# Performance work log

Measured on AMD Instinct MI355X. Metric: run time of the kernel, lower is better.

## Reference

```python
import jax, jax.numpy as jnp
import numpy as np

EPS = 1e-4  # BatchNorm2d eps from source


def binarize(x):
    # brevitas 1-bit quant: sign(x) with sign(0)=+1; straight-through (clipped) estimator
    y = jnp.clip(x, -1.0, 1.0)
    q = jnp.where(x >= 0, 1.0, -1.0).astype(x.dtype)
    return y + jax.lax.stop_gradient(q - y)


def bn(x, g, b, m, v):
    inv = g / jnp.sqrt(v + EPS)
    return x * inv[None, :, None, None] + (b - m * inv)[None, :, None, None]


def conv(x, w, pad):
    return jax.lax.conv_general_dilated(
        x, w, window_strides=(1, 1), padding=[(pad, pad), (pad, pad)],
        dimension_numbers=('NCHW', 'OIHW', 'NCHW'))


def conv_mod(x, w1, bn1, w3, bn3):
    # conv1x1(binary W) -> BN -> binarize act -> conv3x3(binary W) -> BN -> binarize act
    x = conv(x, binarize(w1), 0)
    x = binarize(bn(x, *bn1))
    x = conv(x, binarize(w3), 1)
    x = binarize(bn(x, *bn3))
    return x


def maxpool2(x):
    return jax.lax.reduce_window(x, -jnp.inf, jax.lax.max,
                                 (1, 1, 2, 2), (1, 1, 2, 2), 'VALID')


def setup_inputs() -> dict:
    key = jax.random.key(0)
    ks = jax.random.split(key, 24)
    B, Cin, down, up, H, W = 16, 256, 64, 256, 56, 56
    d = {
        'x':   jax.random.normal(ks[0], (B, Cin, H, W), jnp.float32),
        'w11': jax.random.normal(ks[1], (down, Cin, 1, 1), jnp.float32) * 0.1,
        'w31': jax.random.normal(ks[2], (up, down, 3, 3), jnp.float32) * 0.1,
        'w12': jax.random.normal(ks[3], (down, up, 1, 1), jnp.float32) * 0.1,
        'w32': jax.random.normal(ks[4], (up, down, 3, 3), jnp.float32) * 0.1,
    }
    # BatchNorm params (inference stats): gamma, beta, running mean, running var
    for i, (tag, c) in enumerate([('11', down), ('31', up), ('12', down), ('32', up)]):
        d['g' + tag] = jax.random.uniform(ks[5 + 4 * i], (c,), jnp.float32, 0.5, 1.5)
        d['b' + tag] = jax.random.normal(ks[6 + 4 * i], (c,), jnp.float32) * 0.1
        d['m' + tag] = jax.random.normal(ks[7 + 4 * i], (c,), jnp.float32) * 0.1
        d['v' + tag] = jax.random.uniform(ks[8 + 4 * i], (c,), jnp.float32, 0.5, 1.5)
    return d


def reference(x, w11, w31, w12, w32,
              g11, b11, m11, v11, g31, b31, m31, v31,
              g12, b12, m12, v12, g32, b32, m32, v32):
    h = conv_mod(x, w11, (g11, b11, m11, v11), w31, (g31, b31, m31, v31))
    r = conv_mod(h, w12, (g12, b12, m12, v12), w32, (g32, b32, m32, v32))
    s = binarize(h + r)          # quant_add: re-binarize the residual sum
    return maxpool2(s)           # MaxPool2d(2)
```

## Files before the change

### kernel.cpp

```cpp
#include <hip/hip_runtime.h>
#include <stdint.h>

#pragma clang fp contract(off)


#define HW_   3136
#define NPIX  50176

#define OFF_W31B   0
#define OFF_W12B   18432
#define OFF_W32B   20480
#define OFF_IV11   38912
#define OFF_IV31   39424
#define OFF_IV12   41472
#define OFF_IV32   41984
#define OFF_SGNT   44032
#define OFF_A1     109568
#define OFF_A2     510976
#define OFF_H      912384
#define OFF_S      2518016

__device__ inline float2 mk_ivbt(float g, float b, float m, float v) {
    float inv  = __fdiv_rn(g, __fsqrt_rn(__fadd_rn(v, 1e-4f)));
    float beta = __fsub_rn(b, __fmul_rn(m, inv));
    return make_float2(inv, beta);
}

__global__ __launch_bounds__(256) void k0_all(
    const float* __restrict__ w11, const float* __restrict__ w31,
    const float* __restrict__ w12, const float* __restrict__ w32,
    const float* __restrict__ g11, const float* __restrict__ b11,
    const float* __restrict__ m11, const float* __restrict__ v11,
    const float* __restrict__ g31, const float* __restrict__ b31,
    const float* __restrict__ m31, const float* __restrict__ v31,
    const float* __restrict__ g12, const float* __restrict__ b12,
    const float* __restrict__ m12, const float* __restrict__ v12,
    const float* __restrict__ g32, const float* __restrict__ b32,
    const float* __restrict__ m32, const float* __restrict__ v32,
    uint64_t* __restrict__ W31b, uint64_t* __restrict__ W12b,
    uint64_t* __restrict__ W32b,
    float2* __restrict__ iv11, float2* __restrict__ iv31,
    float2* __restrict__ iv12, float2* __restrict__ iv32,
    float* __restrict__ sgnT)
{
    int blk = blockIdx.x;
    if (blk < 1216) {
        int wid = blk * 4 + (threadIdx.x >> 6);
        int l = threadIdx.x & 63;
        if (wid < 2304) {
            int co = wid / 9, tap = wid % 9;
            uint64_t bits = __ballot(w31[(co * 64 + l) * 9 + tap] >= 0.f);
            if (l == 0) W31b[wid] = bits;
        } else if (wid < 4608) {
            int i = wid - 2304;
            int co = i / 9, tap = i % 9;
            uint64_t bits = __ballot(w32[(co * 64 + l) * 9 + tap] >= 0.f);
            if (l == 0) W32b[i] = bits;
        } else if (wid < 4864) {
            int i = wid - 4608;
            int co = i >> 2, k = i & 3;
            uint64_t bits = __ballot(w12[co * 256 + k * 64 + l] >= 0.f);
            if (l == 0) W12b[i] = bits;
        }
    } else if (blk < 1219) {
        int i = (blk - 1216) * 256 + threadIdx.x;
        if (i < 64)        iv11[i]       = mk_ivbt(g11[i],       b11[i],       m11[i],       v11[i]);
        else if (i < 320)  iv31[i - 64]  = mk_ivbt(g31[i - 64],  b31[i - 64],  m31[i - 64],  v31[i - 64]);
        else if (i < 384)  iv12[i - 320] = mk_ivbt(g12[i - 320], b12[i - 320], m12[i - 320], v12[i - 320]);
        else if (i < 640)  iv32[i - 384] = mk_ivbt(g32[i - 384], b32[i - 384], m32[i - 384], v32[i - 384]);
    } else {
        int t = (blk - 1219) * 256 + threadIdx.x;
        int j = t >> 8, ci = t & 255;
        sgnT[ci * 64 + j] = (w11[t] >= 0.f) ? 1.0f : -1.0f;
    }
}

__global__ __launch_bounds__(256) void k1_conv1(
    const float* __restrict__ x, const float* __restrict__ sgnT,
    const float2* __restrict__ ivbt, unsigned char* __restrict__ A1)
{
    const int l = threadIdx.x & 63;
    const int wv = __builtin_amdgcn_readfirstlane(threadIdx.x >> 6);
    const int blk = blockIdx.x;
    const int half = blk & 1;
    const int g = half * 4 + wv;
    const int P = (blk >> 1) * 256 + l * 4;
    const int bl = P / HW_;
    const int pxl = P - bl * HW_;
    const float* xp = x + (size_t)bl * (256 * HW_) + pxl;
    const float* sg = sgnT + g * 8;

    float acc[8][4];
#pragma unroll
    for (int j = 0; j < 8; ++j)
#pragma unroll
        for (int p = 0; p < 4; ++p) acc[j][p] = 0.0f;

    for (int ci = 0; ci < 256; ci += 8) {
        float4 xv[8];
#pragma unroll
        for (int k = 0; k < 8; ++k)
            xv[k] = *(const float4*)(xp + (size_t)(ci + k) * HW_);
#pragma unroll
        for (int k = 0; k < 8; ++k) {
            const float* s = sg + (ci + k) * 64;
#pragma unroll
            for (int j = 0; j < 8; ++j) {
                acc[j][0] = __builtin_fmaf(s[j], xv[k].x, acc[j][0]);
                acc[j][1] = __builtin_fmaf(s[j], xv[k].y, acc[j][1]);
                acc[j][2] = __builtin_fmaf(s[j], xv[k].z, acc[j][2]);
                acc[j][3] = __builtin_fmaf(s[j], xv[k].w, acc[j][3]);
            }
        }
    }

    unsigned bp0 = 0, bp1 = 0, bp2 = 0, bp3 = 0;
#pragma unroll
    for (int j = 0; j < 8; ++j) {
        float2 ib = ivbt[g * 8 + j];
        bp0 |= (__fadd_rn(__fmul_rn(acc[j][0], ib.x), ib.y) >= 0.0f) ? (1u << j) : 0u;
        bp1 |= (__fadd_rn(__fmul_rn(acc[j][1], ib.x), ib.y) >= 0.0f) ? (1u << j) : 0u;
        bp2 |= (__fadd_rn(__fmul_rn(acc[j][2], ib.x), ib.y) >= 0.0f) ? (1u << j) : 0u;
        bp3 |= (__fadd_rn(__fmul_rn(acc[j][3], ib.x), ib.y) >= 0.0f) ? (1u << j) : 0u;
    }
    unsigned char* a = A1 + (size_t)P * 8 + g;
    a[0]  = (unsigned char)bp0;
    a[8]  = (unsigned char)bp1;
    a[16] = (unsigned char)bp2;
    a[24] = (unsigned char)bp3;
}

template <bool MERGE, bool DO_K3>
__global__ __launch_bounds__(256) void k_conv3c(
    const uint64_t* __restrict__ A, const uint64_t* __restrict__ Wb,
    const float2* __restrict__ ivbt, const uint64_t* __restrict__ Hin,
    uint64_t* __restrict__ Out,
    const uint64_t* __restrict__ W12b, const float2* __restrict__ iv12,
    unsigned short* __restrict__ A2)
{
    __shared__ uint64_t tile[4 * 58];
    __shared__ uint64_t sh4[4][64];
    const int l = threadIdx.x & 63;
    const int wv = threadIdx.x >> 6;
    const int wvu = __builtin_amdgcn_readfirstlane(wv);
    const int chunk = blockIdx.x;
    const int b = chunk / 49;
    const int hw0 = (chunk % 49) * 64;
    const int r0 = hw0 / 56;
    const int o  = hw0 % 56;
    const int rfirst = r0 - 1;

    {
        int idx = threadIdx.x;
        if (idx < 4 * 58) {
            int rr = idx / 58, cc = idx % 58;
            int gh = rfirst + rr, gw = cc - 1;
            uint64_t v = 0;
            if ((unsigned)gh < 56u && (unsigned)gw < 56u)
                v = A[b * HW_ + gh * 56 + gw];
            tile[idx] = v;
        }
    }
    __syncthreads();

    const int inrow2 = (l >= 56 - o) ? 1 : 0;
    const int w = o + l - (inrow2 ? 56 : 0);
    const int row = r0 + inrow2;
    const int rbase = inrow2 * 58;

    uint64_t a[9], m[9];
    int nv = 0;
#pragma unroll
    for (int dr = 0; dr < 3; ++dr)
#pragma unroll
        for (int dc = 0; dc < 3; ++dc) {
            int t = dr * 3 + dc;
            a[t] = tile[rbase + dr * 58 + w + dc];
            bool ok = ((unsigned)(row + dr - 1) < 56u) &&
                      ((unsigned)(w + dc - 1) < 56u);
            m[t] = ok ? ~0ull : 0ull;
            nv += ok;
        }
    const int base = 64 * nv;

    const uint64_t* wbase = Wb + wvu * 64 * 9;
    const float2*   ivb   = ivbt + wvu * 64;

    uint64_t bits = 0;
#pragma unroll 4
    for (int jo = 0; jo < 64; ++jo) {
        const uint64_t* wq = wbase + jo * 9;
        int s = 0;
#pragma unroll
        for (int t = 0; t < 9; ++t)
            s += (int)__popcll((a[t] ^ wq[t]) & m[t]);
        int y = base - 2 * s;
        float2 ib = ivb[jo];
        float val = __fadd_rn(__fmul_rn((float)y, ib.x), ib.y);
        bits |= (uint64_t)(val >= 0.0f) << jo;
    }

    size_t oidx = (size_t)wv * NPIX + (size_t)(b * HW_) + hw0 + l;
    if (MERGE) bits |= Hin[oidx];
    Out[oidx] = bits;

    if (DO_K3) {
        sh4[wv][l] = bits;
        __syncthreads();
        uint64_t h0 = sh4[0][l], h1 = sh4[1][l], h2 = sh4[2][l], h3 = sh4[3][l];
        unsigned bits16 = 0;
#pragma unroll
        for (int jj = 0; jj < 16; ++jj) {
            int cq = wvu * 16 + jj;
            const uint64_t* wq = W12b + cq * 4;
            int s = (int)(__popcll(h0 ^ wq[0]) + __popcll(h1 ^ wq[1]) +
                          __popcll(h2 ^ wq[2]) + __popcll(h3 ^ wq[3]));
            int y = 256 - 2 * s;
            float2 ibq = iv12[cq];
            float val = __fadd_rn(__fmul_rn((float)y, ibq.x), ibq.y);
            bits16 |= (val >= 0.0f) ? (1u << jj) : 0u;
        }
        A2[(size_t)(b * HW_ + hw0 + l) * 4 + wv] = (unsigned short)bits16;
    }
}

__global__ __launch_bounds__(256) void k4b_pool(
    const uint64_t* __restrict__ S, float* __restrict__ out)
{
    int o = blockIdx.x * 256 + threadIdx.x;
    int ow = o % 28;
    int t = o / 28;
    int oh = t % 28; t /= 28;
    int co = t & 255;
    int b  = t >> 8;
    int k = co >> 6, j = co & 63;
    const uint64_t* Sk = S + (size_t)k * NPIX + (size_t)(b * HW_) + (2 * oh) * 56 + 2 * ow;
    uint64_t s = Sk[0] | Sk[1] | Sk[56] | Sk[57];
    out[o] = ((s >> j) & 1) ? 1.0f : -1.0f;
}

extern "C" void kernel_launch(void* const* d_in, const int* in_sizes, int n_in,
                              void* d_out, int out_size, void* d_ws, size_t ws_size,
                              hipStream_t stream)
{
    const float* x   = (const float*)d_in[0];
    const float* w11 = (const float*)d_in[1];
    const float* w31 = (const float*)d_in[2];
    const float* w12 = (const float*)d_in[3];
    const float* w32 = (const float*)d_in[4];
    const float* g11 = (const float*)d_in[5];
    const float* b11 = (const float*)d_in[6];
    const float* m11 = (const float*)d_in[7];
    const float* v11 = (const float*)d_in[8];
    const float* g31 = (const float*)d_in[9];
    const float* b31 = (const float*)d_in[10];
    const float* m31 = (const float*)d_in[11];
    const float* v31 = (const float*)d_in[12];
    const float* g12 = (const float*)d_in[13];
    const float* b12 = (const float*)d_in[14];
    const float* m12 = (const float*)d_in[15];
    const float* v12 = (const float*)d_in[16];
    const float* g32 = (const float*)d_in[17];
    const float* b32 = (const float*)d_in[18];
    const float* m32 = (const float*)d_in[19];
    const float* v32 = (const float*)d_in[20];

    char* ws = (char*)d_ws;
    uint64_t* W31b = (uint64_t*)(ws + OFF_W31B);
    uint64_t* W12b = (uint64_t*)(ws + OFF_W12B);
    uint64_t* W32b = (uint64_t*)(ws + OFF_W32B);
    float2* iv11 = (float2*)(ws + OFF_IV11);
    float2* iv31 = (float2*)(ws + OFF_IV31);
    float2* iv12 = (float2*)(ws + OFF_IV12);
    float2* iv32 = (float2*)(ws + OFF_IV32);
    float*  sgnT = (float*)(ws + OFF_SGNT);
    uint64_t* A1 = (uint64_t*)(ws + OFF_A1);
    uint64_t* A2 = (uint64_t*)(ws + OFF_A2);
    uint64_t* Hb = (uint64_t*)(ws + OFF_H);
    uint64_t* Sb = (uint64_t*)(ws + OFF_S);

    k0_all<<<dim3(1283), dim3(256), 0, stream>>>(
        w11, w31, w12, w32,
        g11, b11, m11, v11, g31, b31, m31, v31,
        g12, b12, m12, v12, g32, b32, m32, v32,
        W31b, W12b, W32b, iv11, iv31, iv12, iv32, sgnT);

    k1_conv1<<<dim3(392), dim3(256), 0, stream>>>(x, sgnT, iv11, (unsigned char*)A1);

    k_conv3c<false, true><<<dim3(784), dim3(256), 0, stream>>>(
        A1, W31b, iv31, (const uint64_t*)nullptr, Hb,
        W12b, iv12, (unsigned short*)A2);

    k_conv3c<true, false><<<dim3(784), dim3(256), 0, stream>>>(
        A2, W32b, iv32, Hb, Sb,
        (const uint64_t*)nullptr, (const float2*)nullptr, (unsigned short*)nullptr);

    k4b_pool<<<dim3(12544), dim3(256), 0, stream>>>(Sb, (float*)d_out);
}
```

Baseline: 116.0 us.

## Retile conv1x1 kernel to 32 channels x 2 pixels per thread with double-buffered loads

The 1x1 binary-weight conv kernel now has each thread compute 32 output channels for 2 pixels instead of 8 channels for 4 pixels. Blocks shrink to 128 threads (two waves, each covering half of the 64 output channels), which removes the duplicate reads of x across blocks. Channel loads are software-pipelined with two register buffers to overlap memory with FMAs, and results are written as 32-bit words instead of bytes. The larger per-thread accumulator set and launch_bounds(128,1) raise register use, and the grid keeps 392 blocks of only 2 waves each, so GPU occupancy drops sharply.

```diff
diff --git a/kernel.cpp b/kernel.cpp
--- a/kernel.cpp
+++ b/kernel.cpp
@@ -75,59 +75,61 @@
     }
 }
 
-__global__ __launch_bounds__(256) void k1_conv1(
+__global__ __launch_bounds__(128, 1) void k1_conv1(
     const float* __restrict__ x, const float* __restrict__ sgnT,
-    const float2* __restrict__ ivbt, unsigned char* __restrict__ A1)
+    const float2* __restrict__ ivbt, uint32_t* __restrict__ A1)
 {
     const int l = threadIdx.x & 63;
-    const int wv = __builtin_amdgcn_readfirstlane(threadIdx.x >> 6);
+    const int half = __builtin_amdgcn_readfirstlane(threadIdx.x >> 6);
     const int blk = blockIdx.x;
-    const int half = blk & 1;
-    const int g = half * 4 + wv;
-    const int P = (blk >> 1) * 256 + l * 4;
+    const int P = blk * 128 + l * 2;
     const int bl = P / HW_;
     const int pxl = P - bl * HW_;
     const float* xp = x + (size_t)bl * (256 * HW_) + pxl;
-    const float* sg = sgnT + g * 8;
-
-    float acc[8][4];
-#pragma unroll
-    for (int j = 0; j < 8; ++j)
-#pragma unroll
-        for (int p = 0; p < 4; ++p) acc[j][p] = 0.0f;
-
-    for (int ci = 0; ci < 256; ci += 8) {
-        float4 xv[8];
-#pragma unroll
-        for (int k = 0; k < 8; ++k)
-            xv[k] = *(const float4*)(xp + (size_t)(ci + k) * HW_);
-#pragma unroll
-        for (int k = 0; k < 8; ++k) {
-            const float* s = sg + (ci + k) * 64;
-#pragma unroll
-            for (int j = 0; j < 8; ++j) {
-                acc[j][0] = __builtin_fmaf(s[j], xv[k].x, acc[j][0]);
-                acc[j][1] = __builtin_fmaf(s[j], xv[k].y, acc[j][1]);
-                acc[j][2] = __builtin_fmaf(s[j], xv[k].z, acc[j][2]);
-                acc[j][3] = __builtin_fmaf(s[j], xv[k].w, acc[j][3]);
-            }
-        }
-    }
-
-    unsigned bp0 = 0, bp1 = 0, bp2 = 0, bp3 = 0;
-#pragma unroll
-    for (int j = 0; j < 8; ++j) {
-        float2 ib = ivbt[g * 8 + j];
+    const float* sg = sgnT + half * 32;
+
+    float acc[32][2];
+#pragma unroll
+    for (int j = 0; j < 32; ++j) { acc[j][0] = 0.0f; acc[j][1] = 0.0f; }
+
+    float2 bufA[8], bufB[8];
+
+#define PF(B, CI0)                                                          \
+    _Pragma("unroll")                                                       \
+    for (int k = 0; k < 8; ++k)                                             \
+        B[k] = *(const float2*)(xp + (size_t)((CI0) + k) * HW_);
+
+#define COMP(B, CI0)                                                        \
+    _Pragma("unroll")                                                       \
+    for (int k = 0; k < 8; ++k) {                                           \
+        const float* s_ = sg + ((CI0) + k) * 64;                            \
+        _Pragma("unroll")                                                   \
+        for (int j = 0; j < 32; ++j) {                                      \
+            acc[j][0] = __builtin_fmaf(s_[j], B[k].x, acc[j][0]);           \
+            acc[j][1] = __builtin_fmaf(s_[j], B[k].y, acc[j][1]);           \
+        }                                                                   \
+    }
+
+    PF(bufA, 0)
+    for (int cb = 0; cb < 256; cb += 16) {
+        PF(bufB, cb + 8)
+        COMP(bufA, cb)
+        if (cb + 16 < 256) { PF(bufA, cb + 16) }
+        COMP(bufB, cb + 8)
+    }
+#undef PF
+#undef COMP
+
+    uint32_t bp0 = 0, bp1 = 0;
+#pragma unroll
+    for (int j = 0; j < 32; ++j) {
+        float2 ib = ivbt[half * 32 + j];
         bp0 |= (__fadd_rn(__fmul_rn(acc[j][0], ib.x), ib.y) >= 0.0f) ? (1u << j) : 0u;
         bp1 |= (__fadd_rn(__fmul_rn(acc[j][1], ib.x), ib.y) >= 0.0f) ? (1u << j) : 0u;
-        bp2 |= (__fadd_rn(__fmul_rn(acc[j][2], ib.x), ib.y) >= 0.0f) ? (1u << j) : 0u;
-        bp3 |= (__fadd_rn(__fmul_rn(acc[j][3], ib.x), ib.y) >= 0.0f) ? (1u << j) : 0u;
-    }
-    unsigned char* a = A1 + (size_t)P * 8 + g;
-    a[0]  = (unsigned char)bp0;
-    a[8]  = (unsigned char)bp1;
-    a[16] = (unsigned char)bp2;
-    a[24] = (unsigned char)bp3;
+    }
+    uint32_t* a = A1 + (size_t)P * 2 + half;
+    a[0] = bp0;
+    a[2] = bp1;
 }
 
 template <bool MERGE, bool DO_K3>
@@ -285,7 +287,7 @@
         g12, b12, m12, v12, g32, b32, m32, v32,
         W31b, W12b, W32b, iv11, iv31, iv12, iv32, sgnT);
 
-    k1_conv1<<<dim3(392), dim3(256), 0, stream>>>(x, sgnT, iv11, (unsigned char*)A1);
+    k1_conv1<<<dim3(392), dim3(128), 0, stream>>>(x, sgnT, iv11, (uint32_t*)A1);
 
     k_conv3c<false, true><<<dim3(784), dim3(256), 0, stream>>>(
         A1, W31b, iv31, (const uint64_t*)nullptr, Hb,
```

Result: slower. 194.8 us (+67.9%).

## Store packed activation bit-planes in planar layout for coalesced writes

Applied to the files above, without the earlier changes.

The packed binary activations A1 (8 byte-planes) and A2 (4 short-planes) change from pixel-interleaved to plane-major layout. The conv1 kernel now writes one 32-bit word per thread covering four consecutive pixels, and conv3 writes shorts contiguously across lanes. The goal is to remove strided sub-word stores. In exchange, the conv3 tile loader now gathers 8 or 4 separate planar loads per pixel instead of one 64-bit load.

```diff
diff --git a/kernel.cpp b/kernel.cpp
--- a/kernel.cpp
+++ b/kernel.cpp
@@ -123,16 +123,13 @@
         bp2 |= (__fadd_rn(__fmul_rn(acc[j][2], ib.x), ib.y) >= 0.0f) ? (1u << j) : 0u;
         bp3 |= (__fadd_rn(__fmul_rn(acc[j][3], ib.x), ib.y) >= 0.0f) ? (1u << j) : 0u;
     }
-    unsigned char* a = A1 + (size_t)P * 8 + g;
-    a[0]  = (unsigned char)bp0;
-    a[8]  = (unsigned char)bp1;
-    a[16] = (unsigned char)bp2;
-    a[24] = (unsigned char)bp3;
-}
-
-template <bool MERGE, bool DO_K3>
+    unsigned word = bp0 | (bp1 << 8) | (bp2 << 16) | (bp3 << 24);
+    *(unsigned*)(A1 + (size_t)g * NPIX + P) = word;
+}
+
+template <bool MERGE, bool DO_K3, bool IN_U8>
 __global__ __launch_bounds__(256) void k_conv3c(
-    const uint64_t* __restrict__ A, const uint64_t* __restrict__ Wb,
+    const void* __restrict__ Ain, const uint64_t* __restrict__ Wb,
     const float2* __restrict__ ivbt, const uint64_t* __restrict__ Hin,
     uint64_t* __restrict__ Out,
     const uint64_t* __restrict__ W12b, const float2* __restrict__ iv12,
@@ -156,8 +153,20 @@
             int rr = idx / 58, cc = idx % 58;
             int gh = rfirst + rr, gw = cc - 1;
             uint64_t v = 0;
-            if ((unsigned)gh < 56u && (unsigned)gw < 56u)
-                v = A[b * HW_ + gh * 56 + gw];
+            if ((unsigned)gh < 56u && (unsigned)gw < 56u) {
+                size_t px = (size_t)b * HW_ + gh * 56 + gw;
+                if (IN_U8) {
+                    const unsigned char* Ab = (const unsigned char*)Ain;
+#pragma unroll
+                    for (int g = 0; g < 8; ++g)
+                        v |= (uint64_t)Ab[(size_t)g * NPIX + px] << (8 * g);
+                } else {
+                    const unsigned short* Ab = (const unsigned short*)Ain;
+#pragma unroll
+                    for (int q = 0; q < 4; ++q)
+                        v |= (uint64_t)Ab[(size_t)q * NPIX + px] << (16 * q);
+                }
+            }
             tile[idx] = v;
         }
     }
@@ -220,7 +229,7 @@
             float val = __fadd_rn(__fmul_rn((float)y, ibq.x), ibq.y);
             bits16 |= (val >= 0.0f) ? (1u << jj) : 0u;
         }
-        A2[(size_t)(b * HW_ + hw0 + l) * 4 + wv] = (unsigned short)bits16;
+        A2[(size_t)wv * NPIX + (size_t)(b * HW_) + hw0 + l] = (unsigned short)bits16;
     }
 }
 
@@ -274,8 +283,8 @@
     float2* iv12 = (float2*)(ws + OFF_IV12);
     float2* iv32 = (float2*)(ws + OFF_IV32);
     float*  sgnT = (float*)(ws + OFF_SGNT);
-    uint64_t* A1 = (uint64_t*)(ws + OFF_A1);
-    uint64_t* A2 = (uint64_t*)(ws + OFF_A2);
+    unsigned char*  A1 = (unsigned char*)(ws + OFF_A1);
+    unsigned short* A2 = (unsigned short*)(ws + OFF_A2);
     uint64_t* Hb = (uint64_t*)(ws + OFF_H);
     uint64_t* Sb = (uint64_t*)(ws + OFF_S);
 
@@ -285,14 +294,14 @@
         g12, b12, m12, v12, g32, b32, m32, v32,
         W31b, W12b, W32b, iv11, iv31, iv12, iv32, sgnT);
 
-    k1_conv1<<<dim3(392), dim3(256), 0, stream>>>(x, sgnT, iv11, (unsigned char*)A1);
-
-    k_conv3c<false, true><<<dim3(784), dim3(256), 0, stream>>>(
-        A1, W31b, iv31, (const uint64_t*)nullptr, Hb,
-        W12b, iv12, (unsigned short*)A2);
-
-    k_conv3c<true, false><<<dim3(784), dim3(256), 0, stream>>>(
-        A2, W32b, iv32, Hb, Sb,
+    k1_conv1<<<dim3(392), dim3(256), 0, stream>>>(x, sgnT, iv11, A1);
+
+    k_conv3c<false, true, true><<<dim3(784), dim3(256), 0, stream>>>(
+        (const void*)A1, W31b, iv31, (const uint64_t*)nullptr, Hb,
+        W12b, iv12, A2);
+
+    k_conv3c<true, false, false><<<dim3(784), dim3(256), 0, stream>>>(
+        (const void*)A2, W32b, iv32, Hb, Sb,
         (const uint64_t*)nullptr, (const float2*)nullptr, (unsigned short*)nullptr);
 
     k4b_pool<<<dim3(12544), dim3(256), 0, stream>>>(Sb, (float*)d_out);
```

Result: slower. 118.9 us (+2.5%).
